# Performance work log

Hardware: AMD Instinct MI355X
Metric: run time of the kernel (lower is better)

Reference implementation:

```python
import jax, jax.numpy as jnp
import numpy as np

# Constant from livnium.kernel.constants (assumed scalar; value taken as 1.0).
K_O = 1.0
EPS = 1e-12  # F.normalize default eps

B, D, C = 16384, 1024, 3
F_DIM = D + 10  # features = h_final (D) + 10 scalar features


def setup_inputs() -> dict:
    key = jax.random.key(0)
    ks = jax.random.split(key, 8)
    s1 = 1.0 / np.sqrt(F_DIM)
    return {
        "h_final": jax.random.normal(ks[0], (B, D), jnp.float32),
        "v_p": jax.random.normal(ks[1], (B, D), jnp.float32),
        "v_h": jax.random.normal(ks[2], (B, D), jnp.float32),
        "neutral_dir": jax.random.normal(ks[3], (D,), jnp.float32),
        "neutral_scale": jnp.array(1.0, jnp.float32),
        "w1": jax.random.normal(ks[4], (F_DIM, F_DIM), jnp.float32) * s1,
        "b1": jnp.zeros((F_DIM,), jnp.float32),
        "w2": jax.random.normal(ks[5], (C, F_DIM), jnp.float32) * s1,
        "b2": jnp.zeros((C,), jnp.float32),
    }


def _normalize(x, axis):
    n = jnp.linalg.norm(x, axis=axis, keepdims=True)
    return x / jnp.maximum(n, EPS)


def reference(h_final, v_p, v_h, neutral_dir, neutral_scale, w1, b1, w2, b2):
    v_p_n = _normalize(v_p, -1)                      # [B, D]
    v_h_n = _normalize(v_h, -1)                      # [B, D]
    nd_n = _normalize(neutral_dir, 0)                # [D]

    # alignment(): cosine of the unit vectors == batched dot product.
    align = jnp.sum(v_p_n * v_h_n, axis=-1, keepdims=True)        # [B, 1]
    opp = jnp.sum(-v_p_n * v_h_n, axis=-1, keepdims=True)          # [B, 1]
    align_neutral_p = neutral_scale * jnp.sum(v_p_n * nd_n, axis=-1, keepdims=True)
    align_neutral_h = neutral_scale * jnp.sum(v_h_n * nd_n, axis=-1, keepdims=True)

    energy = K_O * ((1.0 + align) * 0.5)
    expose_neg = (1.0 - align) * 0.5
    dist_p_h = jnp.linalg.norm(v_h - v_p, axis=-1, keepdims=True)
    r_p = jnp.linalg.norm(v_p, axis=-1, keepdims=True)
    r_h = jnp.linalg.norm(v_h, axis=-1, keepdims=True)
    r_final = jnp.linalg.norm(h_final, axis=-1, keepdims=True)

    features = jnp.concatenate(
        [h_final, align, opp, energy, expose_neg, dist_p_h,
         r_p, r_h, r_final, align_neutral_p, align_neutral_h], axis=-1)  # [B, D+10]

    hidden = jax.nn.relu(features @ w1.T + b1)
    logits = hidden @ w2.T + b2                      # [B, C]
    return logits
```

## Files before the change

### kernel.cpp

```cpp
#include <hip/hip_runtime.h>
#include <cstdint>
#include <cstddef>

#define B_ROWS 16384
#define D_DIM  1024
#define F_REAL 1034
#define N2     1280
#define NBLK   80
#define K2     1056
#define KT_N   33
#define EPSN   1e-12f

#define LDS_RF_OFF   65536
#define LDS_TOTAL    134400

typedef __bf16 bf16x8 __attribute__((ext_vector_type(8)));
typedef float  f32x4  __attribute__((ext_vector_type(4)));
typedef unsigned short u16;
typedef unsigned int   u32;

__device__ __forceinline__ u16 f2bf(float f) {
    __bf16 b = (__bf16)f;
    return __builtin_bit_cast(u16, b);
}

__global__ __launch_bounds__(256)
void prep_kernel(const float* __restrict__ vp,
                 const float* __restrict__ vh, const float* __restrict__ nd,
                 const float* __restrict__ nsp, u16* __restrict__ Ascal)
{
    const int tid  = threadIdx.x;
    const int lane = tid & 63;
    const int wg   = blockIdx.x * 4 + (tid >> 6);
    const int r0   = wg * 4;

    const float4* ndp = (const float4*)nd;
    float4 n[4];
    #pragma unroll
    for (int c = 0; c < 4; ++c) n[c] = ndp[lane + c * 64];
    const float ns = nsp[0];

    float s_nn = 0.f;
    #pragma unroll
    for (int c = 0; c < 4; ++c)
        s_nn += n[c].x*n[c].x + n[c].y*n[c].y + n[c].z*n[c].z + n[c].w*n[c].w;
    #pragma unroll
    for (int m = 32; m >= 1; m >>= 1) s_nn += __shfl_xor(s_nn, m, 64);
    const float nnc = fmaxf(sqrtf(s_nn), EPSN);

    float4 P[2][4], Q[2][4];

#define LOADR(st, r)                                                          \
    do {                                                                      \
        const float4* vpp = (const float4*)(vp + (size_t)(r) * D_DIM);        \
        const float4* vhp = (const float4*)(vh + (size_t)(r) * D_DIM);        \
        _Pragma("unroll")                                                     \
        for (int c = 0; c < 4; ++c) P[st][c] = vpp[lane + c * 64];            \
        _Pragma("unroll")                                                     \
        for (int c = 0; c < 4; ++c) Q[st][c] = vhp[lane + c * 64];            \
    } while (0)

    LOADR(0, r0);
    #pragma unroll
    for (int i = 0; i < 4; ++i) {
        const int st = i & 1;
        if (i + 1 < 4) LOADR(((i + 1) & 1), r0 + i + 1);
        __builtin_amdgcn_sched_barrier(0);

        float s_pp = 0.f, s_hh = 0.f, s_pv = 0.f;
        float s_dd = 0.f, s_pn = 0.f, s_hn = 0.f;
        #pragma unroll
        for (int c = 0; c < 4; ++c) {
            float4 p = P[st][c], q = Q[st][c], nn = n[c];
            s_pp += p.x*p.x + p.y*p.y + p.z*p.z + p.w*p.w;
            s_hh += q.x*q.x + q.y*q.y + q.z*q.z + q.w*q.w;
            s_pv += p.x*q.x + p.y*q.y + p.z*q.z + p.w*q.w;
            float dx = q.x-p.x, dy = q.y-p.y, dz = q.z-p.z, dw = q.w-p.w;
            s_dd += dx*dx + dy*dy + dz*dz + dw*dw;
            s_pn += p.x*nn.x + p.y*nn.y + p.z*nn.z + p.w*nn.w;
            s_hn += q.x*nn.x + q.y*nn.y + q.z*nn.z + q.w*nn.w;
        }

        #pragma unroll
        for (int m = 32; m >= 1; m >>= 1) {
            s_pp += __shfl_xor(s_pp, m, 64);
            s_hh += __shfl_xor(s_hh, m, 64);
            s_pv += __shfl_xor(s_pv, m, 64);
            s_dd += __shfl_xor(s_dd, m, 64);
            s_pn += __shfl_xor(s_pn, m, 64);
            s_hn += __shfl_xor(s_hn, m, 64);
        }

        if (lane == 0) {
            float np_ = sqrtf(s_pp), nh_ = sqrtf(s_hh);
            float npc = fmaxf(np_, EPSN), nhc = fmaxf(nh_, EPSN);
            float align = s_pv / (npc * nhc);
            u16 fo[32];
            fo[0] = f2bf(align);
            fo[1] = f2bf(-align);
            fo[2] = f2bf(0.5f * (1.0f + align));
            fo[3] = f2bf(0.5f * (1.0f - align));
            fo[4] = f2bf(sqrtf(s_dd));
            fo[5] = f2bf(np_);
            fo[6] = f2bf(nh_);
            fo[7] = 0;
            fo[8] = f2bf(ns * s_pn / (npc * nnc));
            fo[9] = f2bf(ns * s_hn / (nhc * nnc));
            #pragma unroll
            for (int k = 10; k < 32; ++k) fo[k] = 0;
            u16* arow = Ascal + (size_t)(r0 + i) * 32;
            #pragma unroll
            for (int k = 0; k < 4; ++k)
                *(uint4*)(arow + k * 8) = *(uint4*)(fo + k * 8);
        }
    }
#undef LOADR
}

__global__ __launch_bounds__(256)
void convw_kernel(const float* __restrict__ w1, u16* __restrict__ Bm2)
{
    const int o = blockIdx.x * 256 + threadIdx.x;
    const int col  = o & 15;
    int t = o >> 4;
    const int quad = t & 3;
    t >>= 2;
    const int nblk = t % NBLK;
    const int kt   = t / NBLK;
    const int n = nblk * 16 + col;
    const int k = kt * 32 + quad * 8;

    u16 v[8];
    if (n < F_REAL && k + 7 < F_REAL) {
        const float* src = w1 + (size_t)n * F_REAL + k;
        #pragma unroll
        for (int e = 0; e < 8; e += 2) {
            float2 f = *(const float2*)(src + e);
            v[e]   = f2bf(f.x);
            v[e+1] = f2bf(f.y);
        }
    } else {
        #pragma unroll
        for (int e = 0; e < 8; ++e) {
            float f = (n < F_REAL && k + e < F_REAL)
                        ? w1[(size_t)n * F_REAL + k + e] : 0.0f;
            v[e] = f2bf(f);
        }
    }
    *(uint4*)(Bm2 + (size_t)o * 8) = *(uint4*)v;
}

__global__ __launch_bounds__(256, 1)
void gemm_kernel(const float* __restrict__ h, const u16* __restrict__ Ascal,
                 const u16* __restrict__ Bm2, const float* __restrict__ b1,
                 const float* __restrict__ w2, const float* __restrict__ b2,
                 float* __restrict__ out)
{
    extern __shared__ u16 smem[];
    u16*   panel = smem;
    float* rf    = (float*)(smem + LDS_RF_OFF);
    float* comb  = rf + 64;

    const int tid  = threadIdx.x;
    const int lane = tid & 63;
    const int wv   = tid >> 6;
    const int col  = lane & 15;
    const int quad = lane >> 4;
    const int bm   = blockIdx.x;

    {
        const float* hblk = h + (size_t)bm * 64 * D_DIM;
        const int halfsel = tid & 1;
        const int chunkid = tid >> 1;
        #pragma unroll 2
        for (int jb = 0; jb < 8; ++jb) {
            float4 v[8];
            #pragma unroll
            for (int u = 0; u < 8; ++u)
                v[u] = *(const float4*)(hblk + (size_t)(jb*8+u)*D_DIM + tid*4);
            #pragma unroll
            for (int u = 0; u < 8; ++u) {
                const int j = jb*8 + u;
                ushort4 o;
                o.x = f2bf(v[u].x); o.y = f2bf(v[u].y);
                o.z = f2bf(v[u].z); o.w = f2bf(v[u].w);
                *(ushort4*)(panel + j*1024 + ((chunkid ^ (j&7))*8) + halfsel*4) = o;
            }
        }
    }
    __syncthreads();

    {
        const int r = wv*16 + (lane >> 2);
        const int q = lane & 3;
        float ssq = 0.f;
        #pragma unroll
        for (int c = 0; c < 32; ++c) {
            const int cc = q*32 + ((c + (lane >> 2)) & 31);
            uint4 tch = *(const uint4*)(panel + r*1024 + cc*8);
            u32 wd[4] = {tch.x, tch.y, tch.z, tch.w};
            #pragma unroll
            for (int e = 0; e < 4; ++e) {
                float lo = __uint_as_float(wd[e] << 16);
                float hi = __uint_as_float(wd[e] & 0xFFFF0000u);
                ssq += lo*lo + hi*hi;
            }
        }
        ssq += __shfl_xor(ssq, 1, 64);
        ssq += __shfl_xor(ssq, 2, 64);
        if (q == 0) rf[r] = sqrtf(ssq);
    }
    __syncthreads();

    u16 rfb[4];
    #pragma unroll
    for (int i = 0; i < 4; ++i) rfb[i] = f2bf(rf[i*16 + col]);

    const int xmask = col & 7;
    int arow[4];
    #pragma unroll
    for (int i = 0; i < 4; ++i) arow[i] = (i*16 + col) * 1024;

    float cacc[3][4][4];
    #pragma unroll
    for (int cls = 0; cls < 3; ++cls)
        #pragma unroll
        for (int mi = 0; mi < 4; ++mi)
            #pragma unroll
            for (int r = 0; r < 4; ++r) cacc[cls][mi][r] = 0.f;

    for (int bnp = 0; bnp < 5; ++bnp) {
        const int nblk0 = bnp*16 + wv*4;
        float bias[4], w20[4], w21[4], w22[4];
        #pragma unroll
        for (int ni = 0; ni < 4; ++ni) {
            const int n = (nblk0 + ni)*16 + col;
            const bool vok = n < F_REAL;
            bias[ni] = vok ? b1[n] : 0.f;
            w20[ni]  = vok ? w2[n] : 0.f;
            w21[ni]  = vok ? w2[F_REAL + n] : 0.f;
            w22[ni]  = vok ? w2[2*F_REAL + n] : 0.f;
        }
        f32x4 acc[4][4];
        #pragma unroll
        for (int i = 0; i < 4; ++i)
            #pragma unroll
            for (int j = 0; j < 4; ++j)
                acc[i][j] = (f32x4){0.f, 0.f, 0.f, 0.f};

        uint4 avA[4], bvA[4], avB[4], bvB[4], avC[4], bvC[4];

#define LOADF(AV, BV, kt, TAIL)                                               \
    do {                                                                      \
        if (TAIL) {                                                           \
            _Pragma("unroll")                                                 \
            for (int i = 0; i < 4; ++i)                                       \
                AV[i] = *(const uint4*)(Ascal +                               \
                         (size_t)(bm*64 + i*16 + col)*32 + quad*8);           \
        } else {                                                              \
            _Pragma("unroll")                                                 \
            for (int i = 0; i < 4; ++i)                                       \
                AV[i] = *(const uint4*)(panel + arow[i] +                     \
                         ((((kt)*4 + quad) ^ xmask) * 8));                    \
        }                                                                     \
        _Pragma("unroll")                                                     \
        for (int j = 0; j < 4; ++j)                                           \
            BV[j] = *(const uint4*)(Bm2 +                                     \
                     ((size_t)((kt)*NBLK + nblk0 + j)*64 + lane)*8);          \
    } while (0)

#define COMPUTE(AV, BV, TAIL)                                                 \
    do {                                                                      \
        bf16x8 a[4], b[4];                                                    \
        _Pragma("unroll")                                                     \
        for (int i = 0; i < 4; ++i) {                                         \
            a[i] = __builtin_bit_cast(bf16x8, AV[i]);                         \
            if (TAIL) { if (quad == 0)                                        \
                a[i][7] = __builtin_bit_cast(__bf16, rfb[i]); }               \
        }                                                                     \
        _Pragma("unroll")                                                     \
        for (int j = 0; j < 4; ++j)                                           \
            b[j] = __builtin_bit_cast(bf16x8, BV[j]);                         \
        _Pragma("unroll")                                                     \
        for (int i = 0; i < 4; ++i)                                           \
            _Pragma("unroll")                                                 \
            for (int j = 0; j < 4; ++j)                                       \
                acc[i][j] = __builtin_amdgcn_mfma_f32_16x16x32_bf16(          \
                                a[i], b[j], acc[i][j], 0, 0, 0);              \
    } while (0)

        LOADF(avA, bvA, 0, 0);
        LOADF(avB, bvB, 1, 0);
        for (int it = 0; it < 10; ++it) {
            const int k0 = it * 3;
            LOADF(avC, bvC, k0+2, 0);  COMPUTE(avA, bvA, 0);
            LOADF(avA, bvA, k0+3, 0);  COMPUTE(avB, bvB, 0);
            LOADF(avB, bvB, k0+4, 0);  COMPUTE(avC, bvC, 0);
        }
        LOADF(avC, bvC, 32, 1);  COMPUTE(avA, bvA, 0);
        COMPUTE(avB, bvB, 0);
        COMPUTE(avC, bvC, 1);

        #pragma unroll
        for (int mi = 0; mi < 4; ++mi)
            #pragma unroll
            for (int ni = 0; ni < 4; ++ni)
                #pragma unroll
                for (int r = 0; r < 4; ++r) {
                    float hd = fmaxf(acc[mi][ni][r] + bias[ni], 0.f);
                    cacc[0][mi][r] += hd * w20[ni];
                    cacc[1][mi][r] += hd * w21[ni];
                    cacc[2][mi][r] += hd * w22[ni];
                }
#undef LOADF
#undef COMPUTE
    }

    #pragma unroll
    for (int cls = 0; cls < 3; ++cls)
        #pragma unroll
        for (int mi = 0; mi < 4; ++mi)
            #pragma unroll
            for (int r = 0; r < 4; ++r) {
                float v = cacc[cls][mi][r];
                v += __shfl_xor(v, 8, 64);
                v += __shfl_xor(v, 4, 64);
                v += __shfl_xor(v, 2, 64);
                v += __shfl_xor(v, 1, 64);
                cacc[cls][mi][r] = v;
            }

    if (col == 0) {
        #pragma unroll
        for (int cls = 0; cls < 3; ++cls)
            #pragma unroll
            for (int mi = 0; mi < 4; ++mi)
                #pragma unroll
                for (int r = 0; r < 4; ++r)
                    comb[wv*192 + (mi*16 + quad*4 + r)*3 + cls] = cacc[cls][mi][r];
    }
    __syncthreads();
    if (tid < 192) {
        float s = comb[tid] + comb[192+tid] + comb[384+tid] + comb[576+tid]
                + b2[tid % 3];
        out[(size_t)bm * 192 + tid] = s;
    }
}

extern "C" void kernel_launch(void* const* d_in, const int* in_sizes, int n_in,
                              void* d_out, int out_size, void* d_ws, size_t ws_size,
                              hipStream_t stream)
{
    const float* h  = (const float*)d_in[0];
    const float* vp = (const float*)d_in[1];
    const float* vh = (const float*)d_in[2];
    const float* nd = (const float*)d_in[3];
    const float* ns = (const float*)d_in[4];
    const float* w1 = (const float*)d_in[5];
    const float* b1 = (const float*)d_in[6];
    const float* w2 = (const float*)d_in[7];
    const float* b2 = (const float*)d_in[8];
    float* out = (float*)d_out;

    u16* Ascal = (u16*)d_ws;
    u16* Bm2   = Ascal + (size_t)B_ROWS * 32;

    static bool attr_done = false;
    if (!attr_done) {
        (void)hipFuncSetAttribute((const void*)gemm_kernel,
                                  hipFuncAttributeMaxDynamicSharedMemorySize,
                                  LDS_TOTAL);
        attr_done = true;
    }

    prep_kernel<<<1024, 256, 0, stream>>>(vp, vh, nd, ns, Ascal);
    convw_kernel<<<660, 256, 0, stream>>>(w1, Bm2);
    gemm_kernel<<<256, 256, LDS_TOTAL, stream>>>(h, Ascal, Bm2, b1, w2, b2, out);
}
```

Baseline: 267.7 us.

## Use 8-wave GEMM blocks with wider N passes and padded weight layout

The GEMM block grows from 4 to 8 waves. The N dimension is padded to 96 column blocks, so the loop becomes 3 passes of 32 blocks instead of 5 passes of 16. The panel load, the row-norm computation and the final cross-wave reduction are re-split across 512 threads, and convw writes the weights into the padded layout. This aims to hide memory and MFMA latency with more waves per CU. The cost is roughly 20% more padded MFMA work, and launch bounds of (512,2) tighten the register budget, which could cause spills.

```diff
diff --git a/kernel.cpp b/kernel.cpp
--- a/kernel.cpp
+++ b/kernel.cpp
@@ -5,14 +5,12 @@
 #define B_ROWS 16384
 #define D_DIM  1024
 #define F_REAL 1034
-#define N2     1280
-#define NBLK   80
-#define K2     1056
+#define NBLK2  96
 #define KT_N   33
 #define EPSN   1e-12f
 
 #define LDS_RF_OFF   65536
-#define LDS_TOTAL    134400
+#define LDS_TOTAL    137472
 
 typedef __bf16 bf16x8 __attribute__((ext_vector_type(8)));
 typedef float  f32x4  __attribute__((ext_vector_type(4)));
@@ -125,8 +123,8 @@
     int t = o >> 4;
     const int quad = t & 3;
     t >>= 2;
-    const int nblk = t % NBLK;
-    const int kt   = t / NBLK;
+    const int nblk = t % NBLK2;
+    const int kt   = t / NBLK2;
     const int n = nblk * 16 + col;
     const int k = kt * 32 + quad * 8;
 
@@ -150,7 +148,7 @@
     *(uint4*)(Bm2 + (size_t)o * 8) = *(uint4*)v;
 }
 
-__global__ __launch_bounds__(256, 1)
+__global__ __launch_bounds__(512, 2)
 void gemm_kernel(const float* __restrict__ h, const u16* __restrict__ Ascal,
                  const u16* __restrict__ Bm2, const float* __restrict__ b1,
                  const float* __restrict__ w2, const float* __restrict__ b2,
@@ -171,16 +169,19 @@
     {
         const float* hblk = h + (size_t)bm * 64 * D_DIM;
         const int halfsel = tid & 1;
-        const int chunkid = tid >> 1;
-        #pragma unroll 2
-        for (int jb = 0; jb < 8; ++jb) {
+        const int chunkid = (tid >> 1) & 127;
+        const int rpair   = tid >> 8;
+        #pragma unroll
+        for (int jb = 0; jb < 4; ++jb) {
             float4 v[8];
             #pragma unroll
-            for (int u = 0; u < 8; ++u)
-                v[u] = *(const float4*)(hblk + (size_t)(jb*8+u)*D_DIM + tid*4);
-            #pragma unroll
             for (int u = 0; u < 8; ++u) {
-                const int j = jb*8 + u;
+                const int j = jb*16 + u*2 + rpair;
+                v[u] = *(const float4*)(hblk + (size_t)j*D_DIM + (tid & 255)*4);
+            }
+            #pragma unroll
+            for (int u = 0; u < 8; ++u) {
+                const int j = jb*16 + u*2 + rpair;
                 ushort4 o;
                 o.x = f2bf(v[u].x); o.y = f2bf(v[u].y);
                 o.z = f2bf(v[u].z); o.w = f2bf(v[u].w);
@@ -191,24 +192,28 @@
     __syncthreads();
 
     {
-        const int r = wv*16 + (lane >> 2);
-        const int q = lane & 3;
-        float ssq = 0.f;
-        #pragma unroll
-        for (int c = 0; c < 32; ++c) {
-            const int cc = q*32 + ((c + (lane >> 2)) & 31);
-            uint4 tch = *(const uint4*)(panel + r*1024 + cc*8);
-            u32 wd[4] = {tch.x, tch.y, tch.z, tch.w};
-            #pragma unroll
-            for (int e = 0; e < 4; ++e) {
-                float lo = __uint_as_float(wd[e] << 16);
-                float hi = __uint_as_float(wd[e] & 0xFFFF0000u);
-                ssq += lo*lo + hi*hi;
+        const int s = tid & 15;
+        #pragma unroll
+        for (int sweep = 0; sweep < 2; ++sweep) {
+            const int r = sweep*32 + (tid >> 4);
+            float ssq = 0.f;
+            #pragma unroll
+            for (int c = 0; c < 8; ++c) {
+                uint4 tch = *(const uint4*)(panel + r*1024 + (s + c*16)*8);
+                u32 wd[4] = {tch.x, tch.y, tch.z, tch.w};
+                #pragma unroll
+                for (int e = 0; e < 4; ++e) {
+                    float lo = __uint_as_float(wd[e] << 16);
+                    float hi = __uint_as_float(wd[e] & 0xFFFF0000u);
+                    ssq += lo*lo + hi*hi;
+                }
             }
-        }
-        ssq += __shfl_xor(ssq, 1, 64);
-        ssq += __shfl_xor(ssq, 2, 64);
-        if (q == 0) rf[r] = sqrtf(ssq);
+            ssq += __shfl_xor(ssq, 1, 64);
+            ssq += __shfl_xor(ssq, 2, 64);
+            ssq += __shfl_xor(ssq, 4, 64);
+            ssq += __shfl_xor(ssq, 8, 64);
+            if (s == 0) rf[r] = sqrtf(ssq);
+        }
     }
     __syncthreads();
 
@@ -229,8 +234,8 @@
             #pragma unroll
             for (int r = 0; r < 4; ++r) cacc[cls][mi][r] = 0.f;
 
-    for (int bnp = 0; bnp < 5; ++bnp) {
-        const int nblk0 = bnp*16 + wv*4;
+    for (int bnp = 0; bnp < 3; ++bnp) {
+        const int nblk0 = bnp*32 + wv*4;
         float bias[4], w20[4], w21[4], w22[4];
         #pragma unroll
         for (int ni = 0; ni < 4; ++ni) {
@@ -266,7 +271,7 @@
         _Pragma("unroll")                                                     \
         for (int j = 0; j < 4; ++j)                                           \
             BV[j] = *(const uint4*)(Bm2 +                                     \
-                     ((size_t)((kt)*NBLK + nblk0 + j)*64 + lane)*8);          \
+                     ((size_t)((kt)*NBLK2 + nblk0 + j)*64 + lane)*8);         \
     } while (0)
 
 #define COMPUTE(AV, BV, TAIL)                                                 \
@@ -341,8 +346,9 @@
     }
     __syncthreads();
     if (tid < 192) {
-        float s = comb[tid] + comb[192+tid] + comb[384+tid] + comb[576+tid]
-                + b2[tid % 3];
+        float s = b2[tid % 3];
+        #pragma unroll
+        for (int w = 0; w < 8; ++w) s += comb[w*192 + tid];
         out[(size_t)bm * 192 + tid] = s;
     }
 }
@@ -374,6 +380,6 @@
     }
 
     prep_kernel<<<1024, 256, 0, stream>>>(vp, vh, nd, ns, Ascal);
-    convw_kernel<<<660, 256, 0, stream>>>(w1, Bm2);
-    gemm_kernel<<<256, 256, LDS_TOTAL, stream>>>(h, Ascal, Bm2, b1, w2, b2, out);
-}
+    convw_kernel<<<792, 256, 0, stream>>>(w1, Bm2);
+    gemm_kernel<<<256, 512, LDS_TOTAL, stream>>>(h, Ascal, Bm2, b1, w2, b2, out);
+}
```

After: 277.8 us. +3.8%, slower.
